# Kernel tuning notes

Measured on AMD Instinct MI355X. Metric: run time of the kernel, lower is better.

Reference implementation:

```python
import jax, jax.numpy as jnp
import numpy as np

DIM = 1024
HEADS = 16
HEAD_DIM = DIM // HEADS
K_NEIGH = 64  # local_window, adaptive_window=False
SCALE = 1.0 / np.sqrt(HEAD_DIM)


def setup_inputs() -> dict:
    key = jax.random.key(0)
    ks = jax.random.split(key, 6)
    b, n = 1, 4096
    x = jax.random.normal(ks[0], (b, n, DIM), dtype=jnp.float32)
    cantor_coords = jax.random.uniform(ks[1], (n,), dtype=jnp.float32)
    # torch nn.Linear(dim, 3*dim): weight [3*dim, dim]; we store transposed [dim, 3*dim]
    W_qkv = jax.random.normal(ks[2], (DIM, 3 * DIM), dtype=jnp.float32) * (1.0 / np.sqrt(DIM))
    b_qkv = jax.random.normal(ks[3], (3 * DIM,), dtype=jnp.float32) * 0.01
    W_out = jax.random.normal(ks[4], (DIM, DIM), dtype=jnp.float32) * (1.0 / np.sqrt(DIM))
    b_out = jax.random.normal(ks[5], (DIM,), dtype=jnp.float32) * 0.01
    return {"x": x, "cantor_coords": cantor_coords, "W_qkv": W_qkv,
            "b_qkv": b_qkv, "W_out": W_out, "b_out": b_out}


def _routes(cantor_coords):
    # [n, n] pairwise |c_i - c_j|; k smallest -> top_k of negated distances
    d = jnp.abs(cantor_coords[:, None] - cantor_coords[None, :])
    _, idx = jax.lax.top_k(-d, K_NEIGH)  # [n, k]
    return idx


def reference(x, cantor_coords, W_qkv, b_qkv, W_out, b_out):
    b, n, _ = x.shape
    qkv = x @ W_qkv + b_qkv                          # [b, n, 3*dim]
    qkv = qkv.reshape(b, n, 3, HEADS, HEAD_DIM)
    qkv = jnp.transpose(qkv, (2, 0, 3, 1, 4))        # [3, b, h, n, d]
    q, k, v = qkv[0], qkv[1], qkv[2]

    routes = _routes(cantor_coords)                  # [n, k]
    k_g = k[:, :, routes, :]                         # [b, h, n, k, d]
    v_g = v[:, :, routes, :]
    scores = jnp.einsum('bhqd,bhqkd->bhqk', q, k_g) * SCALE
    attn = jax.nn.softmax(scores, axis=-1)           # dropout p=0 (eval)
    out = jnp.einsum('bhqk,bhqkd->bhqd', attn, v_g)  # [b, h, n, d]
    out = jnp.transpose(out, (0, 2, 1, 3)).reshape(b, n, DIM)
    return out @ W_out + b_out
```

## Files before the change

kernel.cpp:

```cpp
#include <hip/hip_runtime.h>
#include <hip/hip_bf16.h>

typedef _Float16 f16x8 __attribute__((ext_vector_type(8)));
typedef float f32x4 __attribute__((ext_vector_type(4)));
typedef unsigned long long u64;

#define NSEQ 4096
#define DIMM 1024
#define NHEAD 16
#define HD 64
#define NQKV 3072

#define BAR() asm volatile("s_barrier" ::: "memory")

__device__ __forceinline__ f32x4 mfma16(f16x8 a, f16x8 b, f32x4 c) {
  return __builtin_amdgcn_mfma_f32_16x16x32_f16(a, b, c, 0, 0, 0);
}

__device__ __forceinline__ void glds16(const void* g, void* l) {
  __builtin_amdgcn_global_load_lds(
      (const __attribute__((address_space(1))) void*)g,
      (__attribute__((address_space(3))) void*)l, 16, 0, 0);
}

__global__ __launch_bounds__(256) void prep_kernel(
    const float* __restrict__ x, _Float16* __restrict__ xh,
    const float* __restrict__ Wqkv, _Float16* __restrict__ wqkvt,
    const float* __restrict__ Wout, _Float16* __restrict__ woutt,
    const float* __restrict__ cc, int* __restrict__ sorted_idx,
    float* __restrict__ csort) {
  __shared__ __align__(16) char plds[16640];
  const int bid = blockIdx.x, t = threadIdx.x;
  if (bid < 2048) {
    const int i = bid * 256 + t;
    const float4 a = ((const float4*)x)[i * 2];
    const float4 b = ((const float4*)x)[i * 2 + 1];
    f16x8 o = {(_Float16)a.x, (_Float16)a.y, (_Float16)a.z, (_Float16)a.w,
               (_Float16)b.x, (_Float16)b.y, (_Float16)b.z, (_Float16)b.w};
    ((f16x8*)xh)[i] = o;
  } else if (bid < 3072) {
    const bool qkv = bid < 2816;
    const int sub = qkv ? bid - 2048 : bid - 2816;
    const float* W = qkv ? Wqkv : Wout;
    _Float16* Wt = qkv ? wqkvt : woutt;
    const int Nn = qkv ? 3072 : 1024;
    const int k0 = (sub & 15) * 64, n0 = (sub >> 4) * 64;
    float (*tile)[65] = (float(*)[65])plds;
    const int tx = t & 63, ty = t >> 6;
    for (int rr = ty; rr < 64; rr += 4)
      tile[rr][tx] = W[(size_t)(k0 + rr) * Nn + n0 + tx];
    __syncthreads();
    for (int ccn = ty; ccn < 64; ccn += 4)
      Wt[(size_t)(n0 + ccn) * 1024 + k0 + tx] = (_Float16)tile[tx][ccn];
  } else {
    float* sc = (float*)plds;
#pragma unroll
    for (int it = 0; it < 4; ++it) {
      const int i = it * 256 + t;
      ((float4*)sc)[i] = ((const float4*)cc)[i];
    }
    __syncthreads();
    const int elem = (bid - 3072) * 32 + (t >> 3);
    const int s = t & 7;
    const unsigned mybits = __float_as_uint(sc[elem]);
    int cnt = 0;
#pragma unroll 8
    for (int m = 0; m < 512; ++m) {
      const int j = s + (m << 3);
      const unsigned bj = __float_as_uint(sc[j]);
      cnt += (bj < mybits || (bj == mybits && j < elem)) ? 1 : 0;
    }
    cnt += __shfl_xor(cnt, 1);
    cnt += __shfl_xor(cnt, 2);
    cnt += __shfl_xor(cnt, 4);
    if (s == 0) {
      sorted_idx[cnt] = elem;
      csort[cnt] = sc[elem];
    }
  }
}

__global__ __launch_bounds__(256) void mask_kernel(
    const float* __restrict__ csort, const int* __restrict__ sorted_idx,
    unsigned* __restrict__ masks) {
  __shared__ unsigned lm[4][8];
  const int tid = threadIdx.x, lane = tid & 63, wid = tid >> 6;
  const int p = blockIdx.x * 4 + wid;
  int W0 = 64 * (p >> 6) - 64;
  W0 = min(max(W0, 0), NSEQ - 192);
  const float cp = csort[p];
  u64 key[4];
#pragma unroll
  for (int r = 0; r < 3; ++r) {
    const int w = r * 64 + lane;
    const float d = fabsf(csort[W0 + w] - cp);
    key[r] = (((u64)__float_as_uint(d)) << 20) |
             (((u64)(unsigned)sorted_idx[W0 + w]) << 8) | (unsigned)w;
  }
  key[3] = ~0ull;
  if (lane < 8) lm[wid][lane] = 0u;
#pragma unroll
  for (int k = 2; k <= 256; k <<= 1) {
#pragma unroll
    for (int j = k >> 1; j > 0; j >>= 1) {
      if (j >= 64) {
        const int rj = j >> 6;
#pragma unroll
        for (int r = 0; r < 4; ++r) {
          const int rp = r ^ rj;
          if (rp > r) {
            const bool up = (((r * 64) & k) == 0);
            const u64 a = key[r], b2 = key[rp];
            const bool sw = (a > b2) == up;
            key[r] = sw ? b2 : a;
            key[rp] = sw ? a : b2;
          }
        }
      } else {
#pragma unroll
        for (int r = 0; r < 4; ++r) {
          const u64 pv = __shfl_xor(key[r], j);
          const bool up = (((r * 64 + lane) & k) == 0);
          const bool lower = ((lane & j) == 0);
          const bool takemin = (lower == up);
          const u64 mn = key[r] < pv ? key[r] : pv;
          const u64 mx = key[r] < pv ? pv : key[r];
          key[r] = takemin ? mn : mx;
        }
      }
    }
  }
  const unsigned w0 = (unsigned)(key[0] & 0xffu);
  atomicOr(&lm[wid][w0 >> 5], 1u << (w0 & 31u));
  __syncthreads();
  if (lane < 8) masks[p * 8 + lane] = lm[wid][lane];
}

__device__ __forceinline__ f16x8 ldsfrag(const char* base, int r, int g) {
  return *(const f16x8*)(base + r * 128 + ((g ^ (r & 7)) << 4));
}

__device__ __forceinline__ void stage_half(const char* gbase, size_t kb, int t,
                                           char* lds_half, int tid) {
#pragma unroll
  for (int s = 0; s < 2; ++s) {
    const int rel = tid * 16 + s * 8192;
    const int r = rel >> 7;
    const int g = (rel >> 4) & 7;
    const int gg = g ^ (r & 7);
    glds16(gbase + (size_t)r * kb + t * 128 + gg * 16, lds_half + rel);
  }
}

__device__ __forceinline__ void stage_64r(const char* gbase, size_t kb, int t,
                                          char* lds8k, int tid) {
  const int rel = tid * 16;
  const int r = rel >> 7;
  const int g = (rel >> 4) & 7;
  const int gg = g ^ (r & 7);
  glds16(gbase + (size_t)r * kb + t * 128 + gg * 16, lds8k + rel);
}

__device__ __forceinline__ void rd_b3(const char* Bb, int wn, int lr, int kg,
                                      f16x8 (&bf)[3][2]) {
#pragma unroll
  for (int nt = 0; nt < 3; ++nt) {
    bf[nt][0] = ldsfrag(Bb, wn + nt * 16 + lr, kg);
    bf[nt][1] = ldsfrag(Bb, wn + nt * 16 + lr, 4 + kg);
// ... 83 lines not shown
  do_mfma3<0>(af, bf, acc);
  __builtin_amdgcn_s_setprio(0);
  BAR();
  rd_a<1>(A1, wm, lr, kg, af);
  if (!LAST) {
    stage_64r(Ag + 128 * kb, kb, t2, A0 + 16384, tid);
    stage_64r(Ag + 192 * kb, kb, t2, A0 + 24576, tid);
  }
  BAR();
  __builtin_amdgcn_s_setprio(1);
  do_mfma3<1>(af, bf, acc);
  __builtin_amdgcn_s_setprio(0);
  BAR();
  rd_a<2>(A1, wm, lr, kg, af);
  if (!LAST) {
    stage_64r(Bg, kb, t3, B1, tid);
    stage_64r(Bg + 64 * kb, kb, t3, B1 + 8192, tid);
  }
  BAR();
  __builtin_amdgcn_s_setprio(1);
  do_mfma3<2>(af, bf, acc);
  __builtin_amdgcn_s_setprio(0);
  BAR();
  rd_a<3>(A1, wm, lr, kg, af);
  if (!LAST) stage_64r(Bg + 128 * kb, kb, t3, B1 + 16384, tid);
  BAR();
  __builtin_amdgcn_s_setprio(1);
  do_mfma3<3>(af, bf, acc);
  __builtin_amdgcn_s_setprio(0);
  if (!LAST) asm volatile("s_waitcnt vmcnt(3)" ::: "memory");
  BAR();
}

__global__ __launch_bounds__(512, 2) void qkv_gemm192_kernel(
    const _Float16* __restrict__ A, const _Float16* __restrict__ Bt,
    const float* __restrict__ bias, _Float16* __restrict__ C) {
  extern __shared__ char smem[];
  const int NN = 3072;
  const size_t kb = 2048;
  const int tid = threadIdx.x;
  const int lane = tid & 63, wid = tid >> 6;
  const int lr = lane & 15, kg = lane >> 4;
  const int wm = (wid >> 2) * 128, wn = (wid & 3) * 48;
  const int bid = blockIdx.x;
  const int flat = (bid & 7) * 32 + (bid >> 3);
  const int bx = flat >> 4, by = flat & 15;
  const int m0 = bx * 256, n0 = by * 192;
  const char* Ag = (const char*)A + (size_t)m0 * kb;
  const char* Bg = (const char*)Bt + (size_t)n0 * kb;
  char* A0 = smem;
  char* B0 = smem + 65536;
  char* B1 = smem + 65536 + 24576;
  f32x4 acc[8][3] = {};
#pragma unroll
  for (int u = 0; u < 4; ++u)
    stage_64r(Ag + (size_t)(64 * u) * kb, kb, 0, A0 + u * 8192, tid);
#pragma unroll
  for (int u = 0; u < 3; ++u)
    stage_64r(Bg + (size_t)(64 * u) * kb, kb, 0, B0 + u * 8192, tid);
#pragma unroll
  for (int u = 0; u < 3; ++u)
    stage_64r(Bg + (size_t)(64 * u) * kb, kb, 1, B1 + u * 8192, tid);
  asm volatile("s_waitcnt vmcnt(3)" ::: "memory");
  BAR();
#pragma unroll 1
  for (int i = 0; i < 7; ++i)
    ktile_pair192<false>(Ag, Bg, kb, smem, tid, wm, wn, lr, kg, 2 * i + 1,
                         2 * i + 2, 2 * i + 3, acc);
  ktile_pair192<true>(Ag, Bg, kb, smem, tid, wm, wn, lr, kg, 15, 16, 17, acc);
#pragma unroll
  for (int nt = 0; nt < 3; ++nt) {
    const int col = n0 + wn + nt * 16 + lr;
    const float bv = bias[col];
#pragma unroll
    for (int mt = 0; mt < 8; ++mt) {
      const int row0 = m0 + wm + mt * 16 + kg * 4;
#pragma unroll
      for (int rr = 0; rr < 4; ++rr)
        C[(size_t)(row0 + rr) * NN + col] = (_Float16)(acc[mt][nt][rr] + bv);
    }
  }
}

__global__ __launch_bounds__(512, 2) void out_gemm128_kernel(
    const _Float16* __restrict__ A, const _Float16* __restrict__ Bt,
    const float* __restrict__ bias, float* __restrict__ C) {
  extern __shared__ char smem[];
  const size_t kb = 2048;
  const int tid = threadIdx.x;
  const int lane = tid & 63, wid = tid >> 6;
  const int lr = lane & 15, kg = lane >> 4;
  const int wm = (wid >> 2) * 64, wn = (wid & 3) * 32;
  const int bid = blockIdx.x;
  const int flat = (bid & 7) * 32 + (bid >> 3);
  const int bx = flat >> 3, by = flat & 7;
  const int m0 = bx * 128, n0 = by * 128;
  const char* Ag = (const char*)A + (size_t)m0 * kb;
  const char* Bg = (const char*)Bt + (size_t)n0 * kb;
  f32x4 acc[4][2] = {};
  stage_half(Ag, kb, 0, smem, tid);
  stage_half(Bg, kb, 0, smem + 49152, tid);
  stage_half(Ag, kb, 1, smem + 16384, tid);
  stage_half(Bg, kb, 1, smem + 49152 + 16384, tid);
  asm volatile("s_waitcnt vmcnt(4)" ::: "memory");
  BAR();
#pragma unroll
  for (int t = 0; t < 16; ++t) {
    const char* At = smem + (t % 3) * 16384;
    const char* Bb = smem + 49152 + (t % 3) * 16384;
    f16x8 bf[2][2], af[4][2];
#pragma unroll
    for (int nt = 0; nt < 2; ++nt) {
      bf[nt][0] = ldsfrag(Bb, wn + nt * 16 + lr, kg);
      bf[nt][1] = ldsfrag(Bb, wn + nt * 16 + lr, 4 + kg);
    }
#pragma unroll
    for (int m = 0; m < 4; ++m) {
      af[m][0] = ldsfrag(At, wm + m * 16 + lr, kg);
      af[m][1] = ldsfrag(At, wm + m * 16 + lr, 4 + kg);
    }
    if (t < 14) {
      stage_half(Ag, kb, t + 2, smem + ((t + 2) % 3) * 16384, tid);
      stage_half(Bg, kb, t + 2, smem + 49152 + ((t + 2) % 3) * 16384, tid);
    }
    BAR();
    __builtin_amdgcn_s_setprio(1);
#pragma unroll
    for (int m = 0; m < 4; ++m)
#pragma unroll
      for (int nt = 0; nt < 2; ++nt) {
        acc[m][nt] = mfma16(af[m][0], bf[nt][0], acc[m][nt]);
        acc[m][nt] = mfma16(af[m][1], bf[nt][1], acc[m][nt]);
      }
    __builtin_amdgcn_s_setprio(0);
    if (t < 14)
      asm volatile("s_waitcnt vmcnt(4)" ::: "memory");
    else if (t == 14)
      asm volatile("s_waitcnt vmcnt(0)" ::: "memory");
    BAR();
  }
#pragma unroll
  for (int nt = 0; nt < 2; ++nt) {
    const int col = n0 + wn + nt * 16 + lr;
    const float bv = bias[col];
#pragma unroll
    for (int mt = 0; mt < 4; ++mt) {
      const int row0 = m0 + wm + mt * 16 + kg * 4;
#pragma unroll
      for (int rr = 0; rr < 4; ++rr)
        C[(size_t)(row0 + rr) * 1024 + col] = acc[mt][nt][rr] + bv;
    }
  }
}

__global__ __launch_bounds__(256) void attn_kernel(
    const _Float16* __restrict__ qkvh, const unsigned* __restrict__ masks,
    const int* __restrict__ sorted_idx, _Float16* __restrict__ attn_h) {
  __shared__ __align__(128) char sK[24576];
  __shared__ __align__(128) char sV[24576];
  const int flat = (blockIdx.x & 7) * 128 + (blockIdx.x >> 3);
  const int b = flat & 63, h = flat >> 6;
  const int tid = threadIdx.x, lane = tid & 63, wid = tid >> 6;
  const int W0 = min(max(64 * b - 64, 0), NSEQ - 192);
  const int lrow16 = lane & 15, kgrp = lane >> 4;
  int ridx[6];
#pragma unroll
  for (int c = 0; c < 6; ++c)
    ridx[c] = sorted_idx[W0 + c * 32 + wid * 8 + (lane >> 3)];
#pragma unroll
  for (int c = 0; c < 6; ++c) {
    const int o = c * 4096 + wid * 1024 + lane * 16;
    const int row = o >> 7;
    const int inrow = (o & 127) ^ ((row & 7) << 4);
    glds16((const char*)qkvh + (size_t)ridx[c] * 6144 + 2048 + h * 128 + inrow,
           sK + o);
  }
  f16x8 vreg[6];
#pragma unroll
  for (int c = 0; c < 6; ++c) {
    const int o = c * 4096 + wid * 1024 + lane * 16;
    vreg[c] = *(const f16x8*)((const char*)qkvh + (size_t)ridx[c] * 6144 +
                              4096 + h * 128 + (o & 127));
  }
  const int p_base = b * 64 + wid * 16;
  const int orig_q = sorted_idx[p_base + lrow16];
  const char* qp = (const char*)qkvh + (size_t)orig_q * 6144 + h * 128 + kgrp * 16;
  const f16x8 aq0 = *(const f16x8*)qp;
  const f16x8 aq1 = *(const f16x8*)(qp + 64);
  unsigned mb[4];
#pragma unroll
  for (int r = 0; r < 4; ++r) {
    const int p = p_base + kgrp * 4 + r;
    const uint4 wa = *(const uint4*)&masks[p * 8];
    const uint2 wb2 = *(const uint2*)&masks[p * 8 + 4];
    const unsigned wsv[6] = {wa.x, wa.y, wa.z, wa.w, wb2.x, wb2.y};
    unsigned bits = 0;
#pragma unroll
    for (int n = 0; n < 12; ++n)
      bits |= ((wsv[n >> 1] >> (((n & 1) << 4) + lrow16)) & 1u) << n;
    mb[r] = bits;
  }
  const int lrot = lane & 7;
#pragma unroll
  for (int c = 0; c < 6; ++c) {
    const int o = c * 4096 + wid * 1024 + lane * 16;
    const int k = o >> 7;
    const int d0 = (o & 127) >> 1;
#pragma unroll
    for (int ee = 0; ee < 8; ++ee) {
      const int e = (ee + lrot) & 7;
      const int d = d0 + e;
      *(_Float16*)(sV + d * 384 + ((2 * k) ^ ((d & 7) << 4))) = vreg[c][e];
    }
  }
  __syncthreads();
  float sv[12][4];
#pragma unroll
  for (int n = 0; n < 12; ++n) {
    const int j = n * 16 + lrow16;
    const int sw = (j & 7) << 4;
    const char* kr = sK + j * 128;
    const f16x8 b0 = *(const f16x8*)(kr + ((kgrp * 16) ^ sw));
    const f16x8 b1 = *(const f16x8*)(kr + ((64 + kgrp * 16) ^ sw));
    f32x4 a = {};
    a = mfma16(aq0, b0, a);
    a = mfma16(aq1, b1, a);
#pragma unroll
    for (int r = 0; r < 4; ++r)
      sv[n][r] = ((mb[r] >> n) & 1u) ? a[r] * 0.125f : -1e30f;
  }
#pragma unroll
  for (int r = 0; r < 4; ++r) {
    float m = sv[0][r];
#pragma unroll
    for (int n = 1; n < 12; ++n) m = fmaxf(m, sv[n][r]);
    m = fmaxf(m, __shfl_xor(m, 1));
    m = fmaxf(m, __shfl_xor(m, 2));
    m = fmaxf(m, __shfl_xor(m, 4));
    m = fmaxf(m, __shfl_xor(m, 8));
    float s = 0.f;
#pragma unroll
    for (int n = 0; n < 12; ++n) {
      const float e = __expf(sv[n][r] - m);
      sv[n][r] = e;
      s += e;
    }
    s += __shfl_xor(s, 1);
    s += __shfl_xor(s, 2);
    s += __shfl_xor(s, 4);
    s += __shfl_xor(s, 8);
    const float rinv = 1.f / s;
#pragma unroll
    for (int n = 0; n < 12; ++n) sv[n][r] *= rinv;
  }
  __syncthreads();
#pragma unroll
  for (int n = 0; n < 12; ++n) {
#pragma unroll
    for (int r = 0; r < 4; ++r) {
      const int lr = wid * 16 + kgrp * 4 + r;
      const int cb = (n * 16 + lrow16) * 2;
      *(_Float16*)(sK + lr * 384 + (cb ^ ((lr & 7) << 4))) = (_Float16)sv[n][r];
    }
  }
  __syncthreads();
  f32x4 oacc[4] = {};
  const int arow = wid * 16 + lrow16;
  const int swa = (arow & 7) << 4;
#pragma unroll
  for (int kt = 0; kt < 6; ++kt) {
    const int kbo = kt * 64 + kgrp * 16;
    const f16x8 pa = *(const f16x8*)(sK + arow * 384 + (kbo ^ swa));
#pragma unroll
    for (int nt = 0; nt < 4; ++nt) {
      const int d = nt * 16 + lrow16;
      const f16x8 vb = *(const f16x8*)(sV + d * 384 + (kbo ^ ((d & 7) << 4)));
      oacc[nt] = mfma16(pa, vb, oacc[nt]);
    }
  }
#pragma unroll
  for (int r = 0; r < 4; ++r) {
    const int p = p_base + kgrp * 4 + r;
    const int orig = sorted_idx[p];
    _Float16* op = attn_h + (size_t)orig * DIMM + h * 64;
#pragma unroll
    for (int nt = 0; nt < 4; ++nt)
      op[nt * 16 + lrow16] = (_Float16)oacc[nt][r];
  }
}

extern "C" void kernel_launch(void* const* d_in, const int* in_sizes, int n_in,
                              void* d_out, int out_size, void* d_ws, size_t ws_size,
                              hipStream_t stream) {
  const float* x = (const float*)d_in[0];
  const float* cc = (const float*)d_in[1];
  const float* Wqkv = (const float*)d_in[2];
  const float* bqkv = (const float*)d_in[3];
  const float* Wout = (const float*)d_in[4];
  const float* bout = (const float*)d_in[5];
  char* ws = (char*)d_ws;

  _Float16* xh = (_Float16*)(ws + 0);
  _Float16* wqkvt = (_Float16*)(ws + 8388608);
  _Float16* woutt = (_Float16*)(ws + 14680064);
  _Float16* qkvh = (_Float16*)(ws + 16777216);
  _Float16* atnh = (_Float16*)(ws + 41943040);
  int* sidx = (int*)(ws + 50331648);
  float* csort = (float*)(ws + 50348032);
  unsigned* msk = (unsigned*)(ws + 50364416);

  hipFuncSetAttribute((const void*)qkv_gemm192_kernel,
                      hipFuncAttributeMaxDynamicSharedMemorySize, 114688);
  hipFuncSetAttribute((const void*)out_gemm128_kernel,
                      hipFuncAttributeMaxDynamicSharedMemorySize, 98304);

  prep_kernel<<<3200, 256, 0, stream>>>(x, xh, Wqkv, wqkvt, Wout, woutt, cc,
                                        sidx, csort);
  mask_kernel<<<1024, 256, 0, stream>>>(csort, sidx, msk);
  qkv_gemm192_kernel<<<256, 512, 114688, stream>>>(xh, wqkvt, bqkv, qkvh);
  attn_kernel<<<1024, 256, 0, stream>>>(qkvh, msk, sidx, atnh);
  out_gemm128_kernel<<<256, 512, 98304, stream>>>(atnh, woutt, bout,
                                                  (float*)d_out);
}
```

Measured before the change: 101.4 us.

## Fuse all five stages into one cooperative persistent kernel with grid syncs

Replaces the separate prep, mask, QKV GEMM, attention and output GEMM launches with a single cooperative kernel of 256 blocks. Grid-wide syncs separate the stages, and each block loops over the work units of each stage. The aim is to remove launch overhead and inter-kernel gaps. In exchange, every stage is limited to 256 blocks of 512 threads, the attention stage drops from 1024 small blocks to a persistent layout, and grid.sync adds its own cost.

```diff
diff --git a/kernel.cpp b/kernel.cpp
--- a/kernel.cpp
+++ b/kernel.cpp
@@ -1,5 +1,8 @@
 #include <hip/hip_runtime.h>
 #include <hip/hip_bf16.h>
+#include <hip/hip_cooperative_groups.h>
+
+namespace cg = cooperative_groups;
 
 typedef _Float16 f16x8 __attribute__((ext_vector_type(8)));
 typedef float f32x4 __attribute__((ext_vector_type(4)));
@@ -7,8 +10,6 @@
 
 #define NSEQ 4096
 #define DIMM 1024
-#define NHEAD 16
-#define HD 64
 #define NQKV 3072
 
 #define BAR() asm volatile("s_barrier" ::: "memory")
@@ -21,119 +22,6 @@
   __builtin_amdgcn_global_load_lds(
       (const __attribute__((address_space(1))) void*)g,
       (__attribute__((address_space(3))) void*)l, 16, 0, 0);
-}
-
-__global__ __launch_bounds__(256) void prep_kernel(
-    const float* __restrict__ x, _Float16* __restrict__ xh,
-    const float* __restrict__ Wqkv, _Float16* __restrict__ wqkvt,
-    const float* __restrict__ Wout, _Float16* __restrict__ woutt,
-    const float* __restrict__ cc, int* __restrict__ sorted_idx,
-    float* __restrict__ csort) {
-  __shared__ __align__(16) char plds[16640];
-  const int bid = blockIdx.x, t = threadIdx.x;
-  if (bid < 2048) {
-    const int i = bid * 256 + t;
-    const float4 a = ((const float4*)x)[i * 2];
-    const float4 b = ((const float4*)x)[i * 2 + 1];
-    f16x8 o = {(_Float16)a.x, (_Float16)a.y, (_Float16)a.z, (_Float16)a.w,
-               (_Float16)b.x, (_Float16)b.y, (_Float16)b.z, (_Float16)b.w};
-    ((f16x8*)xh)[i] = o;
-  } else if (bid < 3072) {
-    const bool qkv = bid < 2816;
-    const int sub = qkv ? bid - 2048 : bid - 2816;
-    const float* W = qkv ? Wqkv : Wout;
-    _Float16* Wt = qkv ? wqkvt : woutt;
-    const int Nn = qkv ? 3072 : 1024;
-    const int k0 = (sub & 15) * 64, n0 = (sub >> 4) * 64;
-    float (*tile)[65] = (float(*)[65])plds;
-    const int tx = t & 63, ty = t >> 6;
-    for (int rr = ty; rr < 64; rr += 4)
-      tile[rr][tx] = W[(size_t)(k0 + rr) * Nn + n0 + tx];
-    __syncthreads();
-    for (int ccn = ty; ccn < 64; ccn += 4)
-      Wt[(size_t)(n0 + ccn) * 1024 + k0 + tx] = (_Float16)tile[tx][ccn];
-  } else {
-    float* sc = (float*)plds;
-#pragma unroll
-    for (int it = 0; it < 4; ++it) {
-      const int i = it * 256 + t;
-      ((float4*)sc)[i] = ((const float4*)cc)[i];
-    }
-    __syncthreads();
-    const int elem = (bid - 3072) * 32 + (t >> 3);
-    const int s = t & 7;
-    const unsigned mybits = __float_as_uint(sc[elem]);
-    int cnt = 0;
-#pragma unroll 8
-    for (int m = 0; m < 512; ++m) {
-      const int j = s + (m << 3);
-      const unsigned bj = __float_as_uint(sc[j]);
-      cnt += (bj < mybits || (bj == mybits && j < elem)) ? 1 : 0;
-    }
-    cnt += __shfl_xor(cnt, 1);
-    cnt += __shfl_xor(cnt, 2);
-    cnt += __shfl_xor(cnt, 4);
-    if (s == 0) {
-      sorted_idx[cnt] = elem;
-      csort[cnt] = sc[elem];
-    }
-  }
-}
-
-__global__ __launch_bounds__(256) void mask_kernel(
-    const float* __restrict__ csort, const int* __restrict__ sorted_idx,
-    unsigned* __restrict__ masks) {
-  __shared__ unsigned lm[4][8];
-  const int tid = threadIdx.x, lane = tid & 63, wid = tid >> 6;
-  const int p = blockIdx.x * 4 + wid;
-  int W0 = 64 * (p >> 6) - 64;
-  W0 = min(max(W0, 0), NSEQ - 192);
-  const float cp = csort[p];
-  u64 key[4];
-#pragma unroll
-  for (int r = 0; r < 3; ++r) {
-    const int w = r * 64 + lane;
-    const float d = fabsf(csort[W0 + w] - cp);
-    key[r] = (((u64)__float_as_uint(d)) << 20) |
-             (((u64)(unsigned)sorted_idx[W0 + w]) << 8) | (unsigned)w;
-  }
-  key[3] = ~0ull;
-  if (lane < 8) lm[wid][lane] = 0u;
-#pragma unroll
-  for (int k = 2; k <= 256; k <<= 1) {
-#pragma unroll
-    for (int j = k >> 1; j > 0; j >>= 1) {
-      if (j >= 64) {
-        const int rj = j >> 6;
-#pragma unroll
-        for (int r = 0; r < 4; ++r) {
-          const int rp = r ^ rj;
-          if (rp > r) {
-            const bool up = (((r * 64) & k) == 0);
-            const u64 a = key[r], b2 = key[rp];
-            const bool sw = (a > b2) == up;
-            key[r] = sw ? b2 : a;
-            key[rp] = sw ? a : b2;
-          }
-        }
-      } else {
-#pragma unroll
-        for (int r = 0; r < 4; ++r) {
-          const u64 pv = __shfl_xor(key[r], j);
-          const bool up = (((r * 64 + lane) & k) == 0);
-          const bool lower = ((lane & j) == 0);
-          const bool takemin = (lower == up);
-          const u64 mn = key[r] < pv ? key[r] : pv;
-          const u64 mx = key[r] < pv ? pv : key[r];
-          key[r] = takemin ? mn : mx;
-        }
-      }
-    }
-  }
-  const unsigned w0 = (unsigned)(key[0] & 0xffu);
-  atomicOr(&lm[wid][w0 >> 5], 1u << (w0 & 31u));
-  __syncthreads();
-  if (lane < 8) masks[p * 8 + lane] = lm[wid][lane];
 }
 
 __device__ __forceinline__ f16x8 ldsfrag(const char* base, int r, int g) {
@@ -283,260 +171,385 @@
   BAR();
 }
 
-__global__ __launch_bounds__(512, 2) void qkv_gemm192_kernel(
-    const _Float16* __restrict__ A, const _Float16* __restrict__ Bt,
-    const float* __restrict__ bias, _Float16* __restrict__ C) {
+__global__ __launch_bounds__(512, 2) void mega_kernel(
+    const float* __restrict__ x, const float* __restrict__ cc,
+    const float* __restrict__ Wqkv, const float* __restrict__ bqkv,
+    const float* __restrict__ Wout, const float* __restrict__ bout,
+    _Float16* __restrict__ xh, _Float16* __restrict__ wqkvt,
+    _Float16* __restrict__ woutt, _Float16* __restrict__ qkvh,
+    _Float16* __restrict__ atnh, int* __restrict__ sidx,
+    float* __restrict__ csort, unsigned* __restrict__ msk,
+    float* __restrict__ outp) {
   extern __shared__ char smem[];
-  const int NN = 3072;
-  const size_t kb = 2048;
-  const int tid = threadIdx.x;
+  cg::grid_group grid = cg::this_grid();
+  const int blk = blockIdx.x, tid = threadIdx.x;
   const int lane = tid & 63, wid = tid >> 6;
-  const int lr = lane & 15, kg = lane >> 4;
-  const int wm = (wid >> 2) * 128, wn = (wid & 3) * 48;
-  const int bid = blockIdx.x;
-  const int flat = (bid & 7) * 32 + (bid >> 3);
-  const int bx = flat >> 4, by = flat & 15;
-  const int m0 = bx * 256, n0 = by * 192;
-  const char* Ag = (const char*)A + (size_t)m0 * kb;
-  const char* Bg = (const char*)Bt + (size_t)n0 * kb;
-  char* A0 = smem;
-  char* B0 = smem + 65536;
-  char* B1 = smem + 65536 + 24576;
-  f32x4 acc[8][3] = {};
-#pragma unroll
-  for (int u = 0; u < 4; ++u)
-    stage_64r(Ag + (size_t)(64 * u) * kb, kb, 0, A0 + u * 8192, tid);
-#pragma unroll
-  for (int u = 0; u < 3; ++u)
-    stage_64r(Bg + (size_t)(64 * u) * kb, kb, 0, B0 + u * 8192, tid);
-#pragma unroll
-  for (int u = 0; u < 3; ++u)
-    stage_64r(Bg + (size_t)(64 * u) * kb, kb, 1, B1 + u * 8192, tid);
-  asm volatile("s_waitcnt vmcnt(3)" ::: "memory");
-  BAR();
+
 #pragma unroll 1
-  for (int i = 0; i < 7; ++i)
-    ktile_pair192<false>(Ag, Bg, kb, smem, tid, wm, wn, lr, kg, 2 * i + 1,
-                         2 * i + 2, 2 * i + 3, acc);
-  ktile_pair192<true>(Ag, Bg, kb, smem, tid, wm, wn, lr, kg, 15, 16, 17, acc);
-#pragma unroll
-  for (int nt = 0; nt < 3; ++nt) {
-    const int col = n0 + wn + nt * 16 + lr;
-    const float bv = bias[col];
-#pragma unroll
-    for (int mt = 0; mt < 8; ++mt) {
-      const int row0 = m0 + wm + mt * 16 + kg * 4;
-#pragma unroll
-      for (int rr = 0; rr < 4; ++rr)
-        C[(size_t)(row0 + rr) * NN + col] = (_Float16)(acc[mt][nt][rr] + bv);
-    }
-  }
-}
-
-__global__ __launch_bounds__(512, 2) void out_gemm128_kernel(
-    const _Float16* __restrict__ A, const _Float16* __restrict__ Bt,
-    const float* __restrict__ bias, float* __restrict__ C) {
-  extern __shared__ char smem[];
-  const size_t kb = 2048;
-  const int tid = threadIdx.x;
-  const int lane = tid & 63, wid = tid >> 6;
-  const int lr = lane & 15, kg = lane >> 4;
-  const int wm = (wid >> 2) * 64, wn = (wid & 3) * 32;
-  const int bid = blockIdx.x;
-  const int flat = (bid & 7) * 32 + (bid >> 3);
-  const int bx = flat >> 3, by = flat & 7;
-  const int m0 = bx * 128, n0 = by * 128;
-  const char* Ag = (const char*)A + (size_t)m0 * kb;
-  const char* Bg = (const char*)Bt + (size_t)n0 * kb;
-  f32x4 acc[4][2] = {};
-  stage_half(Ag, kb, 0, smem, tid);
-  stage_half(Bg, kb, 0, smem + 49152, tid);
-  stage_half(Ag, kb, 1, smem + 16384, tid);
-  stage_half(Bg, kb, 1, smem + 49152 + 16384, tid);
-  asm volatile("s_waitcnt vmcnt(4)" ::: "memory");
-  BAR();
-#pragma unroll
-  for (int t = 0; t < 16; ++t) {
-    const char* At = smem + (t % 3) * 16384;
-    const char* Bb = smem + 49152 + (t % 3) * 16384;
-    f16x8 bf[2][2], af[4][2];
+  for (int k = 0;; ++k) {
+    const int u = k * 256 + blk;
+    if (u >= 2112) break;
+    if (u < 1024) {
+      const int i = u * 512 + tid;
+      const float4 a = ((const float4*)x)[i * 2];
+      const float4 b = ((const float4*)x)[i * 2 + 1];
+      f16x8 o = {(_Float16)a.x, (_Float16)a.y, (_Float16)a.z, (_Float16)a.w,
+                 (_Float16)b.x, (_Float16)b.y, (_Float16)b.z, (_Float16)b.w};
+      ((f16x8*)xh)[i] = o;
+    } else if (u < 2048) {
+      const int sub0 = u - 1024;
+      const bool isq = sub0 < 768;
+      const int sub = isq ? sub0 : sub0 - 768;
+      const float* W = isq ? Wqkv : Wout;
+      _Float16* Wt = isq ? wqkvt : woutt;
+      const int Nn = isq ? 3072 : 1024;
+      const int k0 = (sub & 15) * 64, n0 = (sub >> 4) * 64;
+      float(*tile)[65] = (float(*)[65])smem;
+      const int tx = tid & 63, ty = tid >> 6;
+#pragma unroll
+      for (int rr = ty; rr < 64; rr += 8)
+        tile[rr][tx] = W[(size_t)(k0 + rr) * Nn + n0 + tx];
+      __syncthreads();
+#pragma unroll
+      for (int cn = ty; cn < 64; cn += 8)
+        Wt[(size_t)(n0 + cn) * 1024 + k0 + tx] = (_Float16)tile[tx][cn];
+    } else {
+      float* sc = (float*)smem;
+#pragma unroll
+      for (int it = 0; it < 2; ++it)
+        ((float4*)sc)[it * 512 + tid] = ((const float4*)cc)[it * 512 + tid];
+      __syncthreads();
+      const int elem = (u - 2048) * 64 + (tid >> 3);
+      const int s = tid & 7;
+      const unsigned mybits = __float_as_uint(sc[elem]);
+      int cnt = 0;
+#pragma unroll 8
+      for (int m = 0; m < 512; ++m) {
+        const int j = s + (m << 3);
+        const unsigned bj = __float_as_uint(sc[j]);
+        cnt += (bj < mybits || (bj == mybits && j < elem)) ? 1 : 0;
+      }
+      cnt += __shfl_xor(cnt, 1);
+      cnt += __shfl_xor(cnt, 2);
+      cnt += __shfl_xor(cnt, 4);
+      if (s == 0) {
+        sidx[cnt] = elem;
+        csort[cnt] = sc[elem];
+      }
+    }
+    __syncthreads();
+  }
+  __threadfence();
+  grid.sync();
+
+  {
+    unsigned* lmw = (unsigned*)smem + wid * 8;
+#pragma unroll 1
+    for (int it = 0; it < 2; ++it) {
+      const int p = it * 2048 + blk * 8 + wid;
+      int W0m = 64 * (p >> 6) - 64;
+      W0m = min(max(W0m, 0), NSEQ - 192);
+      const float cp = csort[p];
+      u64 key[4];
+#pragma unroll
+      for (int r = 0; r < 3; ++r) {
+        const int w = r * 64 + lane;
+        const float d = fabsf(csort[W0m + w] - cp);
+        key[r] = (((u64)__float_as_uint(d)) << 20) |
+                 (((u64)(unsigned)sidx[W0m + w]) << 8) | (unsigned)w;
+      }
+      key[3] = ~0ull;
+      if (lane < 8) lmw[lane] = 0u;
+#pragma unroll
+      for (int kk = 2; kk <= 256; kk <<= 1) {
+#pragma unroll
+        for (int j = kk >> 1; j > 0; j >>= 1) {
+          if (j >= 64) {
+            const int rj = j >> 6;
+#pragma unroll
+            for (int r = 0; r < 4; ++r) {
+              const int rp = r ^ rj;
+              if (rp > r) {
+                const bool up = (((r * 64) & kk) == 0);
+                const u64 a = key[r], b2 = key[rp];
+                const bool sw = (a > b2) == up;
+                key[r] = sw ? b2 : a;
+                key[rp] = sw ? a : b2;
+              }
+            }
+          } else {
+#pragma unroll
+            for (int r = 0; r < 4; ++r) {
+              const u64 pv = __shfl_xor(key[r], j);
+              const bool up = (((r * 64 + lane) & kk) == 0);
+              const bool lower = ((lane & j) == 0);
+              const bool takemin = (lower == up);
+              const u64 mn = key[r] < pv ? key[r] : pv;
+              const u64 mx = key[r] < pv ? pv : key[r];
+              key[r] = takemin ? mn : mx;
+            }
+          }
+        }
+      }
+      const unsigned w0 = (unsigned)(key[0] & 0xffu);
+      atomicOr(&lmw[w0 >> 5], 1u << (w0 & 31u));
+      if (lane < 8) msk[p * 8 + lane] = lmw[lane];
+    }
+  }
+  __syncthreads();
+
+  {
+    const size_t kb = 2048;
+    const int lr = lane & 15, kg = lane >> 4;
+    const int wm = (wid >> 2) * 128, wn = (wid & 3) * 48;
+    const int flat = (blk & 7) * 32 + (blk >> 3);
+    const int bx = flat >> 4, by = flat & 15;
+    const int m0 = bx * 256, n0 = by * 192;
+    const char* Ag = (const char*)xh + (size_t)m0 * kb;
+    const char* Bg = (const char*)wqkvt + (size_t)n0 * kb;
+    char* A0 = smem;
+    char* B0 = smem + 65536;
+    char* B1 = smem + 65536 + 24576;
+    f32x4 acc[8][3] = {};
+#pragma unroll
+    for (int u = 0; u < 4; ++u)
+      stage_64r(Ag + (size_t)(64 * u) * kb, kb, 0, A0 + u * 8192, tid);
+#pragma unroll
+    for (int u = 0; u < 3; ++u)
+      stage_64r(Bg + (size_t)(64 * u) * kb, kb, 0, B0 + u * 8192, tid);
+#pragma unroll
+    for (int u = 0; u < 3; ++u)
+      stage_64r(Bg + (size_t)(64 * u) * kb, kb, 1, B1 + u * 8192, tid);
+    asm volatile("s_waitcnt vmcnt(3)" ::: "memory");
+    BAR();
+#pragma unroll 1
+    for (int i = 0; i < 7; ++i)
+      ktile_pair192<false>(Ag, Bg, kb, smem, tid, wm, wn, lr, kg, 2 * i + 1,
+                           2 * i + 2, 2 * i + 3, acc);
+    ktile_pair192<true>(Ag, Bg, kb, smem, tid, wm, wn, lr, kg, 15, 16, 17, acc);
+#pragma unroll
+    for (int nt = 0; nt < 3; ++nt) {
+      const int col = n0 + wn + nt * 16 + lr;
+      const float bv = bqkv[col];
+#pragma unroll
+      for (int mt = 0; mt < 8; ++mt) {
+        const int row0 = m0 + wm + mt * 16 + kg * 4;
+#pragma unroll
+        for (int rr = 0; rr < 4; ++rr)
+          qkvh[(size_t)(row0 + rr) * NQKV + col] =
+              (_Float16)(acc[mt][nt][rr] + bv);
+      }
+    }
+  }
+  __threadfence();
+  grid.sync();
+
+  {
+    const int lu = wid >> 2, w4 = wid & 3;
+    char* sKa = smem + lu * 49152;
+    char* sVa = sKa + 24576;
+    const int slot = blk * 2 + lu;
+    const int b = slot & 63;
+    const int W0a = min(max(64 * b - 64, 0), NSEQ - 192);
+    const int lr16 = lane & 15, kg4 = lane >> 4;
+    int ridx[6];
+#pragma unroll
+    for (int c = 0; c < 6; ++c)
+      ridx[c] = sidx[W0a + c * 32 + w4 * 8 + (lane >> 3)];
+    const int p_base = b * 64 + w4 * 16;
+    const int orig_q = sidx[p_base + lr16];
+    unsigned mb[4];
+#pragma unroll
+    for (int r = 0; r < 4; ++r) {
+      const int p = p_base + kg4 * 4 + r;
+      const uint4 wa = *(const uint4*)&msk[p * 8];
+      const uint2 wb2 = *(const uint2*)&msk[p * 8 + 4];
+      const unsigned wsv6[6] = {wa.x, wa.y, wa.z, wa.w, wb2.x, wb2.y};
+      unsigned bits = 0;
+#pragma unroll
+      for (int n = 0; n < 12; ++n)
+        bits |= ((wsv6[n >> 1] >> (((n & 1) << 4) + lr16)) & 1u) << n;
+      mb[r] = bits;
+    }
+    const int lrot = lane & 7;
+#pragma unroll 1
+    for (int it = 0; it < 2; ++it) {
+      const int h = it * 8 + (slot >> 6);
+#pragma unroll
+      for (int c = 0; c < 6; ++c) {
+        const int o = c * 4096 + w4 * 1024 + lane * 16;
+        const int row = o >> 7;
+        const int inrow = (o & 127) ^ ((row & 7) << 4);
+        glds16((const char*)qkvh + (size_t)ridx[c] * 6144 + 2048 + h * 128 + inrow,
+               sKa + o);
+      }
+      f16x8 vreg[6];
+#pragma unroll
+      for (int c = 0; c < 6; ++c) {
+        const int o = c * 4096 + w4 * 1024 + lane * 16;
+        vreg[c] = *(const f16x8*)((const char*)qkvh + (size_t)ridx[c] * 6144 +
+                                  4096 + h * 128 + (o & 127));
+      }
+      const char* qp =
+          (const char*)qkvh + (size_t)orig_q * 6144 + h * 128 + kg4 * 16;
+      const f16x8 aq0 = *(const f16x8*)qp;
+      const f16x8 aq1 = *(const f16x8*)(qp + 64);
+#pragma unroll
+      for (int c = 0; c < 6; ++c) {
+        const int o = c * 4096 + w4 * 1024 + lane * 16;
+        const int kk = o >> 7;
+        const int d0 = (o & 127) >> 1;
+#pragma unroll
+        for (int ee = 0; ee < 8; ++ee) {
+          const int e = (ee + lrot) & 7;
+          const int d = d0 + e;
+          *(_Float16*)(sVa + d * 384 + ((2 * kk) ^ ((d & 7) << 4))) = vreg[c][e];
+        }
+      }
+      __syncthreads();
+      float svv[12][4];
+#pragma unroll
+      for (int n = 0; n < 12; ++n) {
+        const int j = n * 16 + lr16;
+        const int sw = (j & 7) << 4;
+        const char* kr = sKa + j * 128;
+        const f16x8 b0 = *(const f16x8*)(kr + ((kg4 * 16) ^ sw));
+        const f16x8 b1 = *(const f16x8*)(kr + ((64 + kg4 * 16) ^ sw));
+        f32x4 a = {};
+        a = mfma16(aq0, b0, a);
+        a = mfma16(aq1, b1, a);
+#pragma unroll
+        for (int r = 0; r < 4; ++r)
+          svv[n][r] = ((mb[r] >> n) & 1u) ? a[r] * 0.125f : -1e30f;
+      }
+#pragma unroll
+      for (int r = 0; r < 4; ++r) {
+        float m = svv[0][r];
+#pragma unroll
+        for (int n = 1; n < 12; ++n) m = fmaxf(m, svv[n][r]);
+        m = fmaxf(m, __shfl_xor(m, 1));
+        m = fmaxf(m, __shfl_xor(m, 2));
+        m = fmaxf(m, __shfl_xor(m, 4));
+        m = fmaxf(m, __shfl_xor(m, 8));
+        float s = 0.f;
+#pragma unroll
+        for (int n = 0; n < 12; ++n) {
+          const float e = __expf(svv[n][r] - m);
+          svv[n][r] = e;
+          s += e;
+        }
+        s += __shfl_xor(s, 1);
+        s += __shfl_xor(s, 2);
+        s += __shfl_xor(s, 4);
+        s += __shfl_xor(s, 8);
+        const float rinv = 1.f / s;
+#pragma unroll
+        for (int n = 0; n < 12; ++n) svv[n][r] *= rinv;
+      }
+      __syncthreads();
+#pragma unroll
+      for (int n = 0; n < 12; ++n) {
+#pragma unroll
+        for (int r = 0; r < 4; ++r) {
+          const int lrw = w4 * 16 + kg4 * 4 + r;
+          const int cb = (n * 16 + lr16) * 2;
+          *(_Float16*)(sKa + lrw * 384 + (cb ^ ((lrw & 7) << 4))) =
+              (_Float16)svv[n][r];
+        }
+      }
+      __syncthreads();
+      f32x4 oacc[4] = {};
+      const int arow = w4 * 16 + lr16;
+      const int swa = (arow & 7) << 4;
+#pragma unroll
+      for (int kt = 0; kt < 6; ++kt) {
+        const int kbo = kt * 64 + kg4 * 16;
+        const f16x8 pa = *(const f16x8*)(sKa + arow * 384 + (kbo ^ swa));
+#pragma unroll
+        for (int nt = 0; nt < 4; ++nt) {
+          const int d = nt * 16 + lr16;
+          const f16x8 vb = *(const f16x8*)(sVa + d * 384 + (kbo ^ ((d & 7) << 4)));
+          oacc[nt] = mfma16(pa, vb, oacc[nt]);
+        }
+      }
+#pragma unroll
+      for (int r = 0; r < 4; ++r) {
+        const int p = p_base + kg4 * 4 + r;
+        const int orig = sidx[p];
+        _Float16* op = atnh + (size_t)orig * DIMM + h * 64;
+#pragma unroll
+        for (int nt = 0; nt < 4; ++nt)
+          op[nt * 16 + lr16] = (_Float16)oacc[nt][r];
+      }
+      __syncthreads();
+    }
+  }
+  __threadfence();
+  grid.sync();
+
+  {
+    const size_t kb = 2048;
+    const int lr = lane & 15, kg = lane >> 4;
+    const int wm = (wid >> 2) * 64, wn = (wid & 3) * 32;
+    const int flat = (blk & 7) * 32 + (blk >> 3);
+    const int bx = flat >> 3, by = flat & 7;
+    const int m0 = bx * 128, n0 = by * 128;
+    const char* Ag = (const char*)atnh + (size_t)m0 * kb;
+    const char* Bg = (const char*)woutt + (size_t)n0 * kb;
+    f32x4 acc[4][2] = {};
+    stage_half(Ag, kb, 0, smem, tid);
+    stage_half(Bg, kb, 0, smem + 49152, tid);
+    stage_half(Ag, kb, 1, smem + 16384, tid);
+    stage_half(Bg, kb, 1, smem + 49152 + 16384, tid);
+    asm volatile("s_waitcnt vmcnt(4)" ::: "memory");
+    BAR();
+#pragma unroll
+    for (int t = 0; t < 16; ++t) {
+      const char* At = smem + (t % 3) * 16384;
+      const char* Bb = smem + 49152 + (t % 3) * 16384;
+      f16x8 bf[2][2], af[4][2];
+#pragma unroll
+      for (int nt = 0; nt < 2; ++nt) {
+        bf[nt][0] = ldsfrag(Bb, wn + nt * 16 + lr, kg);
+        bf[nt][1] = ldsfrag(Bb, wn + nt * 16 + lr, 4 + kg);
+      }
+#pragma unroll
+      for (int m = 0; m < 4; ++m) {
+        af[m][0] = ldsfrag(At, wm + m * 16 + lr, kg);
+        af[m][1] = ldsfrag(At, wm + m * 16 + lr, 4 + kg);
+      }
+      if (t < 14) {
+        stage_half(Ag, kb, t + 2, smem + ((t + 2) % 3) * 16384, tid);
+        stage_half(Bg, kb, t + 2, smem + 49152 + ((t + 2) % 3) * 16384, tid);
+      }
+      BAR();
+      __builtin_amdgcn_s_setprio(1);
+#pragma unroll
+      for (int m = 0; m < 4; ++m)
+#pragma unroll
+        for (int nt = 0; nt < 2; ++nt) {
+          acc[m][nt] = mfma16(af[m][0], bf[nt][0], acc[m][nt]);
+          acc[m][nt] = mfma16(af[m][1], bf[nt][1], acc[m][nt]);
+        }
+      __builtin_amdgcn_s_setprio(0);
+      if (t < 14)
+        asm volatile("s_waitcnt vmcnt(4)" ::: "memory");
+      else if (t == 14)
+        asm volatile("s_waitcnt vmcnt(0)" ::: "memory");
+      BAR();
+    }
 #pragma unroll
     for (int nt = 0; nt < 2; ++nt) {
-      bf[nt][0] = ldsfrag(Bb, wn + nt * 16 + lr, kg);
-      bf[nt][1] = ldsfrag(Bb, wn + nt * 16 + lr, 4 + kg);
-    }
-#pragma unroll
-    for (int m = 0; m < 4; ++m) {
-      af[m][0] = ldsfrag(At, wm + m * 16 + lr, kg);
-      af[m][1] = ldsfrag(At, wm + m * 16 + lr, 4 + kg);
-    }
-    if (t < 14) {
-      stage_half(Ag, kb, t + 2, smem + ((t + 2) % 3) * 16384, tid);
-      stage_half(Bg, kb, t + 2, smem + 49152 + ((t + 2) % 3) * 16384, tid);
-    }
-    BAR();
-    __builtin_amdgcn_s_setprio(1);
-#pragma unroll
-    for (int m = 0; m < 4; ++m)
-#pragma unroll
-      for (int nt = 0; nt < 2; ++nt) {
-        acc[m][nt] = mfma16(af[m][0], bf[nt][0], acc[m][nt]);
-        acc[m][nt] = mfma16(af[m][1], bf[nt][1], acc[m][nt]);
-      }
-    __builtin_amdgcn_s_setprio(0);
-    if (t < 14)
-      asm volatile("s_waitcnt vmcnt(4)" ::: "memory");
-    else if (t == 14)
-      asm volatile("s_waitcnt vmcnt(0)" ::: "memory");
-    BAR();
-  }
-#pragma unroll
-  for (int nt = 0; nt < 2; ++nt) {
-    const int col = n0 + wn + nt * 16 + lr;
-    const float bv = bias[col];
-#pragma unroll
-    for (int mt = 0; mt < 4; ++mt) {
-      const int row0 = m0 + wm + mt * 16 + kg * 4;
-#pragma unroll
-      for (int rr = 0; rr < 4; ++rr)
-        C[(size_t)(row0 + rr) * 1024 + col] = acc[mt][nt][rr] + bv;
-    }
-  }
-}
-
-__global__ __launch_bounds__(256) void attn_kernel(
-    const _Float16* __restrict__ qkvh, const unsigned* __restrict__ masks,
-    const int* __restrict__ sorted_idx, _Float16* __restrict__ attn_h) {
-  __shared__ __align__(128) char sK[24576];
-  __shared__ __align__(128) char sV[24576];
-  const int flat = (blockIdx.x & 7) * 128 + (blockIdx.x >> 3);
-  const int b = flat & 63, h = flat >> 6;
-  const int tid = threadIdx.x, lane = tid & 63, wid = tid >> 6;
-  const int W0 = min(max(64 * b - 64, 0), NSEQ - 192);
-  const int lrow16 = lane & 15, kgrp = lane >> 4;
-  int ridx[6];
-#pragma unroll
-  for (int c = 0; c < 6; ++c)
-    ridx[c] = sorted_idx[W0 + c * 32 + wid * 8 + (lane >> 3)];
-#pragma unroll
-  for (int c = 0; c < 6; ++c) {
-    const int o = c * 4096 + wid * 1024 + lane * 16;
-    const int row = o >> 7;
-    const int inrow = (o & 127) ^ ((row & 7) << 4);
-    glds16((const char*)qkvh + (size_t)ridx[c] * 6144 + 2048 + h * 128 + inrow,
-           sK + o);
-  }
-  f16x8 vreg[6];
-#pragma unroll
-  for (int c = 0; c < 6; ++c) {
-    const int o = c * 4096 + wid * 1024 + lane * 16;
-    vreg[c] = *(const f16x8*)((const char*)qkvh + (size_t)ridx[c] * 6144 +
-                              4096 + h * 128 + (o & 127));
-  }
-  const int p_base = b * 64 + wid * 16;
-  const int orig_q = sorted_idx[p_base + lrow16];
-  const char* qp = (const char*)qkvh + (size_t)orig_q * 6144 + h * 128 + kgrp * 16;
-  const f16x8 aq0 = *(const f16x8*)qp;
-  const f16x8 aq1 = *(const f16x8*)(qp + 64);
-  unsigned mb[4];
-#pragma unroll
-  for (int r = 0; r < 4; ++r) {
-    const int p = p_base + kgrp * 4 + r;
-    const uint4 wa = *(const uint4*)&masks[p * 8];
-    const uint2 wb2 = *(const uint2*)&masks[p * 8 + 4];
-    const unsigned wsv[6] = {wa.x, wa.y, wa.z, wa.w, wb2.x, wb2.y};
-    unsigned bits = 0;
-#pragma unroll
-    for (int n = 0; n < 12; ++n)
-      bits |= ((wsv[n >> 1] >> (((n & 1) << 4) + lrow16)) & 1u) << n;
-    mb[r] = bits;
-  }
-  const int lrot = lane & 7;
-#pragma unroll
-  for (int c = 0; c < 6; ++c) {
-    const int o = c * 4096 + wid * 1024 + lane * 16;
-    const int k = o >> 7;
-    const int d0 = (o & 127) >> 1;
-#pragma unroll
-    for (int ee = 0; ee < 8; ++ee) {
-      const int e = (ee + lrot) & 7;
-      const int d = d0 + e;
-      *(_Float16*)(sV + d * 384 + ((2 * k) ^ ((d & 7) << 4))) = vreg[c][e];
-    }
-  }
-  __syncthreads();
-  float sv[12][4];
-#pragma unroll
-  for (int n = 0; n < 12; ++n) {
-    const int j = n * 16 + lrow16;
-    const int sw = (j & 7) << 4;
-    const char* kr = sK + j * 128;
-    const f16x8 b0 = *(const f16x8*)(kr + ((kgrp * 16) ^ sw));
-    const f16x8 b1 = *(const f16x8*)(kr + ((64 + kgrp * 16) ^ sw));
-    f32x4 a = {};
-    a = mfma16(aq0, b0, a);
-    a = mfma16(aq1, b1, a);
-#pragma unroll
-    for (int r = 0; r < 4; ++r)
-      sv[n][r] = ((mb[r] >> n) & 1u) ? a[r] * 0.125f : -1e30f;
-  }
-#pragma unroll
-  for (int r = 0; r < 4; ++r) {
-    float m = sv[0][r];
-#pragma unroll
-    for (int n = 1; n < 12; ++n) m = fmaxf(m, sv[n][r]);
-    m = fmaxf(m, __shfl_xor(m, 1));
-    m = fmaxf(m, __shfl_xor(m, 2));
-    m = fmaxf(m, __shfl_xor(m, 4));
-    m = fmaxf(m, __shfl_xor(m, 8));
-    float s = 0.f;
-#pragma unroll
-    for (int n = 0; n < 12; ++n) {
-      const float e = __expf(sv[n][r] - m);
-      sv[n][r] = e;
-      s += e;
-    }
-    s += __shfl_xor(s, 1);
-    s += __shfl_xor(s, 2);
-    s += __shfl_xor(s, 4);
-    s += __shfl_xor(s, 8);
-    const float rinv = 1.f / s;
-#pragma unroll
-    for (int n = 0; n < 12; ++n) sv[n][r] *= rinv;
-  }
-  __syncthreads();
-#pragma unroll
-  for (int n = 0; n < 12; ++n) {
-#pragma unroll
-    for (int r = 0; r < 4; ++r) {
-      const int lr = wid * 16 + kgrp * 4 + r;
-      const int cb = (n * 16 + lrow16) * 2;
-      *(_Float16*)(sK + lr * 384 + (cb ^ ((lr & 7) << 4))) = (_Float16)sv[n][r];
-    }
-  }
-  __syncthreads();
-  f32x4 oacc[4] = {};
-  const int arow = wid * 16 + lrow16;
-  const int swa = (arow & 7) << 4;
-#pragma unroll
-  for (int kt = 0; kt < 6; ++kt) {
-    const int kbo = kt * 64 + kgrp * 16;
-    const f16x8 pa = *(const f16x8*)(sK + arow * 384 + (kbo ^ swa));
-#pragma unroll
-    for (int nt = 0; nt < 4; ++nt) {
-      const int d = nt * 16 + lrow16;
-      const f16x8 vb = *(const f16x8*)(sV + d * 384 + (kbo ^ ((d & 7) << 4)));
-      oacc[nt] = mfma16(pa, vb, oacc[nt]);
-    }
-  }
-#pragma unroll
-  for (int r = 0; r < 4; ++r) {
-    const int p = p_base + kgrp * 4 + r;
-    const int orig = sorted_idx[p];
-    _Float16* op = attn_h + (size_t)orig * DIMM + h * 64;
-#pragma unroll
-    for (int nt = 0; nt < 4; ++nt)
-      op[nt * 16 + lrow16] = (_Float16)oacc[nt][r];
+      const int col = n0 + wn + nt * 16 + lr;
+      const float bv = bout[col];
+#pragma unroll
+      for (int mt = 0; mt < 4; ++mt) {
+        const int row0 = m0 + wm + mt * 16 + kg * 4;
+#pragma unroll
+        for (int rr = 0; rr < 4; ++rr)
+          outp[(size_t)(row0 + rr) * 1024 + col] = acc[mt][nt][rr] + bv;
+      }
+    }
   }
 }
 
@@ -559,17 +572,15 @@
   int* sidx = (int*)(ws + 50331648);
   float* csort = (float*)(ws + 50348032);
   unsigned* msk = (unsigned*)(ws + 50364416);
-
-  hipFuncSetAttribute((const void*)qkv_gemm192_kernel,
+  float* outp = (float*)d_out;
+
+  hipFuncSetAttribute((const void*)mega_kernel,
                       hipFuncAttributeMaxDynamicSharedMemorySize, 114688);
-  hipFuncSetAttribute((const void*)out_gemm128_kernel,
-                      hipFuncAttributeMaxDynamicSharedMemorySize, 98304);
-
-  prep_kernel<<<3200, 256, 0, stream>>>(x, xh, Wqkv, wqkvt, Wout, woutt, cc,
-                                        sidx, csort);
-  mask_kernel<<<1024, 256, 0, stream>>>(csort, sidx, msk);
-  qkv_gemm192_kernel<<<256, 512, 114688, stream>>>(xh, wqkvt, bqkv, qkvh);
-  attn_kernel<<<1024, 256, 0, stream>>>(qkvh, msk, sidx, atnh);
-  out_gemm128_kernel<<<256, 512, 98304, stream>>>(atnh, woutt, bout,
-                                                  (float*)d_out);
-}
+
+  void* args[] = {(void*)&x,     (void*)&cc,    (void*)&Wqkv, (void*)&bqkv,
+                  (void*)&Wout,  (void*)&bout,  (void*)&xh,   (void*)&wqkvt,
+                  (void*)&woutt, (void*)&qkvh,  (void*)&atnh, (void*)&sidx,
+                  (void*)&csort, (void*)&msk,   (void*)&outp};
+  hipLaunchCooperativeKernel((const void*)mega_kernel, dim3(256), dim3(512),
+                             args, 114688, stream);
+}
```

New measurement: 351.9 us. 247% more time.

## Fuse neighbor-mask sort into QKV GEMM launch and vectorize weight transpose stores

Applied to the files above, without the earlier changes.

Removes the separate mask_kernel launch by appending 512 extra blocks to the QKV GEMM grid that run the bitonic top-k mask computation. The shared-memory atomicOr mask build is replaced by wave-wide shuffle OR reductions. The prep kernel's weight-transpose writes become 16-byte f16x8 stores instead of scalar half stores. The mask blocks request the GEMM's large dynamic shared memory allocation even though they use none, which may limit how many of them are resident at once and affect scheduling alongside the GEMM blocks.

```diff
diff --git a/kernel.cpp b/kernel.cpp
--- a/kernel.cpp
+++ b/kernel.cpp
@@ -7,8 +7,6 @@
 
 #define NSEQ 4096
 #define DIMM 1024
-#define NHEAD 16
-#define HD 64
 #define NQKV 3072
 
 #define BAR() asm volatile("s_barrier" ::: "memory")
@@ -50,8 +48,15 @@
     for (int rr = ty; rr < 64; rr += 4)
       tile[rr][tx] = W[(size_t)(k0 + rr) * Nn + n0 + tx];
     __syncthreads();
-    for (int ccn = ty; ccn < 64; ccn += 4)
-      Wt[(size_t)(n0 + ccn) * 1024 + k0 + tx] = (_Float16)tile[tx][ccn];
+#pragma unroll
+    for (int it = 0; it < 2; ++it) {
+      const int idx = it * 256 + t;
+      const int row = idx >> 3, seg = idx & 7;
+      f16x8 v;
+#pragma unroll
+      for (int j = 0; j < 8; ++j) v[j] = (_Float16)tile[seg * 8 + j][row];
+      *(f16x8*)&Wt[(size_t)(n0 + row) * 1024 + k0 + seg * 8] = v;
+    }
   } else {
     float* sc = (float*)plds;
 #pragma unroll
@@ -78,62 +83,6 @@
       csort[cnt] = sc[elem];
     }
   }
-}
-
-__global__ __launch_bounds__(256) void mask_kernel(
-    const float* __restrict__ csort, const int* __restrict__ sorted_idx,
-    unsigned* __restrict__ masks) {
-  __shared__ unsigned lm[4][8];
-  const int tid = threadIdx.x, lane = tid & 63, wid = tid >> 6;
-  const int p = blockIdx.x * 4 + wid;
-  int W0 = 64 * (p >> 6) - 64;
-  W0 = min(max(W0, 0), NSEQ - 192);
-  const float cp = csort[p];
-  u64 key[4];
-#pragma unroll
-  for (int r = 0; r < 3; ++r) {
-    const int w = r * 64 + lane;
-    const float d = fabsf(csort[W0 + w] - cp);
-    key[r] = (((u64)__float_as_uint(d)) << 20) |
-             (((u64)(unsigned)sorted_idx[W0 + w]) << 8) | (unsigned)w;
-  }
-  key[3] = ~0ull;
-  if (lane < 8) lm[wid][lane] = 0u;
-#pragma unroll
-  for (int k = 2; k <= 256; k <<= 1) {
-#pragma unroll
-    for (int j = k >> 1; j > 0; j >>= 1) {
-      if (j >= 64) {
-        const int rj = j >> 6;
-#pragma unroll
-        for (int r = 0; r < 4; ++r) {
-          const int rp = r ^ rj;
-          if (rp > r) {
-            const bool up = (((r * 64) & k) == 0);
-            const u64 a = key[r], b2 = key[rp];
-            const bool sw = (a > b2) == up;
-            key[r] = sw ? b2 : a;
-            key[rp] = sw ? a : b2;
-          }
-        }
-      } else {
-#pragma unroll
-        for (int r = 0; r < 4; ++r) {
-          const u64 pv = __shfl_xor(key[r], j);
-          const bool up = (((r * 64 + lane) & k) == 0);
-          const bool lower = ((lane & j) == 0);
-          const bool takemin = (lower == up);
-          const u64 mn = key[r] < pv ? key[r] : pv;
-          const u64 mx = key[r] < pv ? pv : key[r];
-          key[r] = takemin ? mn : mx;
-        }
-      }
-    }
-  }
-  const unsigned w0 = (unsigned)(key[0] & 0xffu);
-  atomicOr(&lm[wid][w0 >> 5], 1u << (w0 & 31u));
-  __syncthreads();
-  if (lane < 8) masks[p * 8 + lane] = lm[wid][lane];
 }
 
 __device__ __forceinline__ f16x8 ldsfrag(const char* base, int r, int g) {
@@ -283,14 +232,90 @@
   BAR();
 }
 
-__global__ __launch_bounds__(512, 2) void qkv_gemm192_kernel(
+__global__ __launch_bounds__(512, 2) void qkvmask_kernel(
     const _Float16* __restrict__ A, const _Float16* __restrict__ Bt,
-    const float* __restrict__ bias, _Float16* __restrict__ C) {
+    const float* __restrict__ bias, _Float16* __restrict__ C,
+    const float* __restrict__ csort, const int* __restrict__ sorted_idx,
+    unsigned* __restrict__ masks) {
   extern __shared__ char smem[];
+  const int tid = threadIdx.x;
+  const int lane = tid & 63, wid = tid >> 6;
+  if (blockIdx.x >= 256) {
+    const int p = (blockIdx.x - 256) * 8 + wid;
+    int W0 = 64 * (p >> 6) - 64;
+    W0 = min(max(W0, 0), NSEQ - 192);
+    const float cp = csort[p];
+    u64 key[4];
+#pragma unroll
+    for (int r = 0; r < 3; ++r) {
+      const int w = r * 64 + lane;
+      const float d = fabsf(csort[W0 + w] - cp);
+      key[r] = (((u64)__float_as_uint(d)) << 20) |
+               (((u64)(unsigned)sorted_idx[W0 + w]) << 8) | (unsigned)w;
+    }
+    key[3] = ~0ull;
+#pragma unroll
+    for (int k = 2; k <= 256; k <<= 1) {
+#pragma unroll
+      for (int j = k >> 1; j > 0; j >>= 1) {
+        if (j >= 64) {
+          const int rj = j >> 6;
+#pragma unroll
+          for (int r = 0; r < 4; ++r) {
+            const int rp = r ^ rj;
+            if (rp > r) {
+              const bool up = (((r * 64) & k) == 0);
+              const u64 a = key[r], b2 = key[rp];
+              const bool sw = (a > b2) == up;
+              key[r] = sw ? b2 : a;
+              key[rp] = sw ? a : b2;
+            }
+          }
+        } else {
+#pragma unroll
+          for (int r = 0; r < 4; ++r) {
+            const u64 pv = __shfl_xor(key[r], j);
+            const bool up = (((r * 64 + lane) & k) == 0);
+            const bool lower = ((lane & j) == 0);
+            const bool takemin = (lower == up);
+            const u64 mn = key[r] < pv ? key[r] : pv;
+            const u64 mx = key[r] < pv ? pv : key[r];
+            key[r] = takemin ? mn : mx;
+          }
+        }
+      }
+    }
+    const unsigned w0 = (unsigned)(key[0] & 0xffu);
+    const unsigned hi = w0 >> 5, bit = 1u << (w0 & 31u);
+    unsigned m0w = hi == 0 ? bit : 0u;
+    unsigned m1w = hi == 1 ? bit : 0u;
+    unsigned m2w = hi == 2 ? bit : 0u;
+    unsigned m3w = hi == 3 ? bit : 0u;
+    unsigned m4w = hi == 4 ? bit : 0u;
+    unsigned m5w = hi == 5 ? bit : 0u;
+#pragma unroll
+    for (int s = 1; s < 64; s <<= 1) {
+      m0w |= __shfl_xor(m0w, s);
+      m1w |= __shfl_xor(m1w, s);
+      m2w |= __shfl_xor(m2w, s);
+      m3w |= __shfl_xor(m3w, s);
+      m4w |= __shfl_xor(m4w, s);
+      m5w |= __shfl_xor(m5w, s);
+    }
+    if (lane < 8) {
+      unsigned val = 0u;
+      val = lane == 0 ? m0w : val;
+      val = lane == 1 ? m1w : val;
+      val = lane == 2 ? m2w : val;
+      val = lane == 3 ? m3w : val;
+      val = lane == 4 ? m4w : val;
+      val = lane == 5 ? m5w : val;
+      masks[p * 8 + lane] = val;
+    }
+    return;
+  }
   const int NN = 3072;
   const size_t kb = 2048;
-  const int tid = threadIdx.x;
-  const int lane = tid & 63, wid = tid >> 6;
   const int lr = lane & 15, kg = lane >> 4;
   const int wm = (wid >> 2) * 128, wn = (wid & 3) * 48;
   const int bid = blockIdx.x;
@@ -444,11 +469,11 @@
     const int p = p_base + kgrp * 4 + r;
     const uint4 wa = *(const uint4*)&masks[p * 8];
     const uint2 wb2 = *(const uint2*)&masks[p * 8 + 4];
-    const unsigned wsv[6] = {wa.x, wa.y, wa.z, wa.w, wb2.x, wb2.y};
+    const unsigned wsv6[6] = {wa.x, wa.y, wa.z, wa.w, wb2.x, wb2.y};
     unsigned bits = 0;
 #pragma unroll
     for (int n = 0; n < 12; ++n)
-      bits |= ((wsv[n >> 1] >> (((n & 1) << 4) + lrow16)) & 1u) << n;
+      bits |= ((wsv6[n >> 1] >> (((n & 1) << 4) + lrow16)) & 1u) << n;
     mb[r] = bits;
   }
   const int lrot = lane & 7;
@@ -509,9 +534,9 @@
   for (int n = 0; n < 12; ++n) {
 #pragma unroll
     for (int r = 0; r < 4; ++r) {
-      const int lr = wid * 16 + kgrp * 4 + r;
+      const int lrw = wid * 16 + kgrp * 4 + r;
       const int cb = (n * 16 + lrow16) * 2;
-      *(_Float16*)(sK + lr * 384 + (cb ^ ((lr & 7) << 4))) = (_Float16)sv[n][r];
+      *(_Float16*)(sK + lrw * 384 + (cb ^ ((lrw & 7) << 4))) = (_Float16)sv[n][r];
     }
   }
   __syncthreads();
@@ -560,15 +585,15 @@
   float* csort = (float*)(ws + 50348032);
   unsigned* msk = (unsigned*)(ws + 50364416);
 
-  hipFuncSetAttribute((const void*)qkv_gemm192_kernel,
+  hipFuncSetAttribute((const void*)qkvmask_kernel,
                       hipFuncAttributeMaxDynamicSharedMemorySize, 114688);
   hipFuncSetAttribute((const void*)out_gemm128_kernel,
                       hipFuncAttributeMaxDynamicSharedMemorySize, 98304);
 
   prep_kernel<<<3200, 256, 0, stream>>>(x, xh, Wqkv, wqkvt, Wout, woutt, cc,
                                         sidx, csort);
-  mask_kernel<<<1024, 256, 0, stream>>>(csort, sidx, msk);
-  qkv_gemm192_kernel<<<256, 512, 114688, stream>>>(xh, wqkvt, bqkv, qkvh);
+  qkvmask_kernel<<<768, 512, 114688, stream>>>(xh, wqkvt, bqkv, qkvh, csort,
+                                               sidx, msk);
   attn_kernel<<<1024, 256, 0, stream>>>(qkvh, msk, sidx, atnh);
   out_gemm128_kernel<<<256, 512, 98304, stream>>>(atnh, woutt, bout,
                                                   (float*)d_out);
```

Measured after the change: 102.0 us. About the same (+0.5%).
